# Kernel tuning notes

Measured on AMD Instinct MI355X. Metric: run time of the kernel, lower is better.

The kernel has to match this reference:

```python
import jax, jax.numpy as jnp
import numpy as np

B, CIN, CH, COUT = 16, 256, 256, 256
RES = 16
E = 32           # embed_dim
NEMB = 1024      # codebook size
NP = 128         # n_phylo_channels (ch - NP == NP)
L = 4            # n_phylolevels
K = 8            # attribute codes per level per kernel
KN = 32          # nonattribute codes per kernel (levels=1)
CP = L * K * E   # 1024 projected phylo channels
CN = KN * E      # 1024 projected nonattr channels
BETA = 0.25
EPS = 1e-5

def conv1x1(x, w, b):
    # x: [B,C,H,W], w: [O,C], b: [O]
    return jnp.einsum('oc,bchw->bohw', w, x) + b[None, :, None, None]

def layernorm_chw(x, w, b):
    # LayerNorm over (C,H,W) per sample, elementwise affine of shape [C,H,W]
    mu = jnp.mean(x, axis=(1, 2, 3), keepdims=True)
    var = jnp.var(x, axis=(1, 2, 3), keepdims=True)
    return (x - mu) * jax.lax.rsqrt(var + EPS) * w[None] + b[None]

def reshape_in(x, levels):
    # [B, E*levels*K', H, W] -> [B, E, K'*H*W, levels]
    Bb, C, H, W = x.shape
    Kp = C // (E * levels)
    x = x.reshape(Bb, E, levels, Kp, H * W)
    x = x.transpose(0, 1, 3, 4, 2)          # [B,E,K',HW,levels]
    return x.reshape(Bb, E, Kp * H * W, levels)

def reshape_out(x, levels):
    # [B, E, K'*HW, levels] -> [B, E*levels*K', RES, RES]
    Bb, Ee, N, Ll = x.shape
    Kp = N // (RES * RES)
    x = x.reshape(Bb, Ee, Kp, RES * RES, Ll)
    x = x.transpose(0, 1, 4, 2, 3)          # [B,E,levels,K',HW]
    return x.reshape(Bb, Ee * Ll * Kp, RES, RES)

def quantize(z, codebook):
    # z: [B, E, N, levels]; codebook: [NEMB, E]
    zp = z.transpose(0, 2, 3, 1)            # [B,N,levels,E]
    flat = zp.reshape(-1, E)
    d = (jnp.sum(flat * flat, axis=1, keepdims=True)
         - 2.0 * flat @ codebook.T
         + jnp.sum(codebook * codebook, axis=1)[None, :])
    idx = jnp.argmin(d, axis=1)
    zq = codebook[idx].reshape(zp.shape)
    sg = jax.lax.stop_gradient
    loss = jnp.mean((sg(zq) - zp) ** 2) + BETA * jnp.mean((zq - sg(zp)) ** 2)
    zq = zp + sg(zq - zp)                   # straight-through
    return zq.transpose(0, 3, 1, 2), loss

def setup_inputs() -> dict:
    key = jax.random.key(0)
    ks = jax.random.split(key, 20)
    s = 0.02
    inp = {
        'x': jax.random.normal(ks[0], (B, CIN, RES, RES), jnp.float32),
        'conv_in_w': jax.random.normal(ks[1], (CH, CIN), jnp.float32) * s,
        'conv_in_b': jnp.zeros((CH,), jnp.float32),
        'ln_p_w': jnp.ones((NP, RES, RES), jnp.float32),
        'ln_p_b': jnp.zeros((NP, RES, RES), jnp.float32),
        'wp_in': jax.random.normal(ks[2], (CP, NP), jnp.float32) * s,
        'bp_in': jnp.zeros((CP,), jnp.float32),
        'wp_out': jax.random.normal(ks[3], (NP, CP), jnp.float32) * s,
        'bp_out': jnp.zeros((NP,), jnp.float32),
        'ln_n_w': jnp.ones((CH - NP, RES, RES), jnp.float32),
        'ln_n_b': jnp.zeros((CH - NP, RES, RES), jnp.float32),
        'wn_in': jax.random.normal(ks[4], (CN, CH - NP), jnp.float32) * s,
        'bn_in': jnp.zeros((CN,), jnp.float32),
        'wn_out': jax.random.normal(ks[5], (CH - NP, CN), jnp.float32) * s,
        'bn_out': jnp.zeros((CH - NP,), jnp.float32),
        'codebook': jax.random.uniform(ks[6], (NEMB, E), jnp.float32,
                                       -1.0 / NEMB, 1.0 / NEMB),
        'conv_out_w': jax.random.normal(ks[7], (COUT, CH), jnp.float32) * s,
        'conv_out_b': jnp.zeros((COUT,), jnp.float32),
    }
    return inp

def reference(x, conv_in_w, conv_in_b, ln_p_w, ln_p_b, wp_in, bp_in,
              wp_out, bp_out, ln_n_w, ln_n_b, wn_in, bn_in, wn_out, bn_out,
              codebook, conv_out_w, conv_out_b):
    silu = jax.nn.silu
    h = conv1x1(silu(x), conv_in_w, conv_in_b)
    h_p, h_n = h[:, :NP], h[:, NP:]
    # phylo branch
    z_p = silu(conv1x1(layernorm_chw(silu(h_p), ln_p_w, ln_p_b), wp_in, bp_in))
    zq_p, loss_p = quantize(reshape_in(z_p, L), codebook)
    hout_p = silu(conv1x1(reshape_out(zq_p, L), wp_out, bp_out))
    # non-attribute branch (anticlassification path)
    z_n = silu(conv1x1(layernorm_chw(silu(h_n), ln_n_w, ln_n_b), wn_in, bn_in))
    zq_n, loss_n = quantize(reshape_in(z_n, 1), codebook)
    hout_n = silu(conv1x1(reshape_out(zq_n, 1), wn_out, bn_out))
    h_cat = jnp.concatenate([hout_p, hout_n], axis=1)
    out = conv1x1(silu(h_cat), conv_out_w, conv_out_b)
    return out, loss_p + loss_n, zq_p
```

## Files before the change

### kernel.cpp

```cpp
#include <hip/hip_runtime.h>
#include <hip/hip_bf16.h>


__device__ __forceinline__ float silu_rw(float x){ return x / (1.f + expf(-x)); }
__device__ __forceinline__ float b2f_rw(__hip_bfloat16 v){ return __bfloat162float(v); }
__device__ __forceinline__ float ldv_rw(const void* p, int i, int f32m){
  if (f32m) return ((const float*)p)[i];
  return b2f_rw(((const __hip_bfloat16*)p)[i]);
}

#define FLAGS_OFF 0
#define LOSS_OFF  4
#define STATS_OFF 8
#define CB32_OFF  128
#define CBN_OFF   32896
#define IDXP_OFF  33984
#define IDXN_OFF  165056
#define R2_OFF    296192
#define R3_OFF    820480
#define R1_OFF    1344768

__global__ __launch_bounds__(256) void detect_rw(const void* cbv, float* flags, float* lossacc){
  __shared__ int bad;
  if (threadIdx.x == 0) bad = 0;
  __syncthreads();
  const unsigned short* u = (const unsigned short*)cbv;
  int local = 0;
  for (int i = threadIdx.x; i < 32768; i += 256){
    unsigned e = (u[i] >> 7) & 0xFF;
    if (e >= 126) local = 1;
  }
  if (local) bad = 1;
  __syncthreads();
  if (threadIdx.x == 0){
    flags[0] = bad ? 1.f : 0.f;
    lossacc[0] = 0.f; lossacc[1] = 0.f;
  }
}

__global__ __launch_bounds__(256) void cbprep_rw(const void* cbv, const float* flags,
                                                 float* cb32, float* cbn){
  const int f32m = (flags[0] != 0.f);
  int j = blockIdx.x * 256 + threadIdx.x;
  if (j < 1024){
    float s = 0.f;
    for (int e = 0; e < 32; ++e){
      float v = ldv_rw(cbv, j*32 + e, f32m);
      cb32[j*32 + e] = v;
      s += v*v;
    }
    cbn[j] = s;
  }
}

template<int KCH, int INMODE, bool OUTSILU, bool ATOMIC, int LEVELS>
__global__ __launch_bounds__(256) void gemm2_rw(
    const float* __restrict__ inF, const float* __restrict__ inF2,
    const void* __restrict__ inV,
    const void* __restrict__ W, const void* __restrict__ biasO,
    const void* __restrict__ sbA, const void* __restrict__ sbB,
    const int* __restrict__ idxin, const float* __restrict__ cb32,
    float* __restrict__ outF, const float* __restrict__ flags,
    int KDIM, int OUTC, int o_off, int b_base, int ib_sub, int ob_sub)
{
  __shared__ float As[32][32];
  __shared__ float Bs[32][68];
  __shared__ int   IdxS[32][32];

  const int f32m = (flags[0] != 0.f);
  const int t  = threadIdx.x;
  const int q0 = (blockIdx.x << 5) + (b_base << 8);
  const int b  = q0 >> 8;
  const int p0 = q0 & 255;
  const int o0 = blockIdx.y << 6;
  const int k0base = blockIdx.z * KCH;
  const int tx = t & 15, ty = t >> 4;
  float acc[4][2] = {};

  const int sch = t >> 3, spx = (t & 7) << 2;

  if constexpr (INMODE == 3){
    #pragma unroll
    for (int j = 0; j < 4; ++j){
      const int p = p0 + spx + j;
      if constexpr (LEVELS == 4){
        const int l = sch >> 3, kp = sch & 7;
        IdxS[sch][spx + j] = idxin[b*8192 + (((kp << 8) + p) << 2) + l];
      } else {
        IdxS[sch][spx + j] = idxin[b*8192 + (sch << 8) + p];
      }
    }
    __syncthreads();
  }

  for (int kc = 0; kc < KCH; kc += 32){
    const int k0 = k0base + kc;
    if constexpr (INMODE == 0){
      const float4 v = *reinterpret_cast<const float4*>(
          &inF[(((b - ib_sub)*KDIM + k0 + sch) << 8) + p0 + spx]);
      *reinterpret_cast<float4*>(&As[sch][spx]) = v;
    } else if constexpr (INMODE == 2){
      if (f32m){
        const float* xf = (const float*)inV;
        float4 v = *reinterpret_cast<const float4*>(&xf[((b*KDIM + k0 + sch) << 8) + p0 + spx]);
        v.x = silu_rw(v.x); v.y = silu_rw(v.y); v.z = silu_rw(v.z); v.w = silu_rw(v.w);
        *reinterpret_cast<float4*>(&As[sch][spx]) = v;
      } else {
        const __hip_bfloat16* xb = (const __hip_bfloat16*)inV;
        const int off = ((b*KDIM + k0 + sch) << 8) + p0 + spx;
        #pragma unroll
        for (int j = 0; j < 4; ++j) As[sch][spx + j] = silu_rw(b2f_rw(xb[off + j]));
      }
    } else if constexpr (INMODE == 3){
      const int e = k0 >> 5;
      #pragma unroll
      for (int j = 0; j < 4; ++j)
        As[sch][spx + j] = cb32[((IdxS[sch][spx + j] & 1023) << 5) + e];
    } else {
      const float* src = (k0 < 128) ? inF : inF2;
      const void* sb   = (k0 < 128) ? sbA : sbB;
      const int kh = k0 & 127;
      const float bb = ldv_rw(sb, kh + sch, f32m);
      float4 v = *reinterpret_cast<const float4*>(&src[((b*128 + kh + sch) << 8) + p0 + spx]);
      v.x = silu_rw(v.x + bb); v.y = silu_rw(v.y + bb);
      v.z = silu_rw(v.z + bb); v.w = silu_rw(v.w + bb);
      *reinterpret_cast<float4*>(&As[sch][spx]) = v;
    }
    if (f32m){
      const float* Wf = (const float*)W;
      #pragma unroll
      for (int r = 0; r < 8; ++r){
        int ii = t + (r << 8); int oo = ii >> 5, cc = ii & 31;
        Bs[cc][oo] = Wf[(o0 + oo)*KDIM + k0 + cc];
      }
    } else {
      const __hip_bfloat16* Wb = (const __hip_bfloat16*)W;
      #pragma unroll
      for (int r = 0; r < 8; ++r){
        int ii = t + (r << 8); int oo = ii >> 5, cc = ii & 31;
        Bs[cc][oo] = b2f_rw(Wb[(o0 + oo)*KDIM + k0 + cc]);
      }
    }
    __syncthreads();
    #pragma unroll
    for (int kk = 0; kk < 32; ++kk){
      const float2 a = *reinterpret_cast<const float2*>(&As[kk][tx << 1]);
      const float4 w = *reinterpret_cast<const float4*>(&Bs[kk][ty << 2]);
      acc[0][0] += w.x*a.x; acc[0][1] += w.x*a.y;
      acc[1][0] += w.y*a.x; acc[1][1] += w.y*a.y;
      acc[2][0] += w.z*a.x; acc[2][1] += w.z*a.y;
      acc[3][0] += w.w*a.x; acc[3][1] += w.w*a.y;
    }
    __syncthreads();
  }
  #pragma unroll
  for (int i = 0; i < 4; ++i){
    const int o = o0 + (ty << 2) + i;
    const int base = (((b - ob_sub)*OUTC + o_off + o) << 8) + p0 + (tx << 1);
    if constexpr (ATOMIC){
      atomicAdd(&outF[base + 0], acc[i][0]);
      atomicAdd(&outF[base + 1], acc[i][1]);
    } else {
      const float bb = ldv_rw(biasO, o, f32m);
      float v0 = acc[i][0] + bb, v1 = acc[i][1] + bb;
      if constexpr (OUTSILU){ v0 = silu_rw(v0); v1 = silu_rw(v1); }
      *reinterpret_cast<float2*>(&outF[base]) = make_float2(v0, v1);
    }
  }
}

__global__ __launch_bounds__(256) void stats_rw(const float* __restrict__ h, float* __restrict__ stats){
  const int b = blockIdx.x >> 1, half = blockIdx.x & 1;
  const float* base = h + ((b*256 + half*128) << 8);
  float s = 0.f, s2 = 0.f;
  for (int i = threadIdx.x; i < 32768; i += 256){
    float a = silu_rw(base[i]);
    s += a; s2 += a*a;
  }
  __shared__ float sh[2][256];
  sh[0][threadIdx.x] = s; sh[1][threadIdx.x] = s2;
  __syncthreads();
  for (int st = 128; st > 0; st >>= 1){
    if (threadIdx.x < st){
      sh[0][threadIdx.x] += sh[0][threadIdx.x + st];
      sh[1][threadIdx.x] += sh[1][threadIdx.x + st];
    }
    __syncthreads();
  }
  if (threadIdx.x == 0){
    float mu  = sh[0][0] * (1.f/32768.f);
    float var = sh[1][0] * (1.f/32768.f) - mu*mu;
    stats[half*32 + b]      = mu;
    stats[half*32 + 16 + b] = 1.f / sqrtf(var + 1e-5f);
  }
}

__global__ __launch_bounds__(256) void ln_rw(const float* __restrict__ h,
    const void* lwp, const void* lbp, const void* lwn, const void* lbn,
    const float* __restrict__ stats, const float* __restrict__ flags,
    float* __restrict__ lnp, float* __restrict__ lnn){
  const int f32m = (flags[0] != 0.f);
  int i = blockIdx.x * 256 + threadIdx.x;
  int b = i >> 16, c = (i >> 8) & 255, p = i & 255;
  float a = silu_rw(h[i]);
  if (c < 128){
    float v = (a - stats[b]) * stats[16 + b] * ldv_rw(lwp, (c << 8) + p, f32m) + ldv_rw(lbp, (c << 8) + p, f32m);
    lnp[((b*128 + c) << 8) + p] = v;
  } else {
    int cc = c - 128;
    float v = (a - stats[32 + b]) * stats[48 + b] * ldv_rw(lwn, (cc << 8) + p, f32m) + ldv_rw(lbn, (cc << 8) + p, f32m);
    lnn[((b*128 + cc) << 8) + p] = v;
  }
}

template<int LEVELS>
__global__ __launch_bounds__(256) void quant_rw(const float* __restrict__ z,
    const float* __restrict__ cb32, const float* __restrict__ cbn,
    int* __restrict__ idxout, float* __restrict__ lossacc, int b_base, int CS){
  __shared__ float4 cbT[2056];
  __shared__ float  cbnS[1056];
  __shared__ float  red[256];

  const int tid = threadIdx.x;
  const int gid = blockIdx.x * 256 + tid;
  const int pt = gid & 7;
  const int vbase = gid >> 3;
  const int halfstride = CS << 12;
  const int vid0 = vbase, vid1 = vbase + halfstride;

  const int bl0 = vid0 >> 13, bl1 = vid1 >> 13;
  const int w = vid0 & 8191;
  int p, cbase;
  if (LEVELS == 4){
    int l = w & 3, n = w >> 2;
    p = n & 255; cbase = (l << 3) + (n >> 8);
  } else {
    p = w & 255; cbase = w >> 8;
  }

  #pragma unroll
  for (int q = 0; q < 4; ++q){
    const int i = tid + (q << 8);
    cbnS[i + (i >> 5)] = cbn[i];
  }

  float4 za[8], zb[8];
  float zn0 = 0.f, zn1 = 0.f;
  const int zoff = ((bl0 << 10) + cbase) << 8;
  const int zoff1 = ((bl1 << 10) + cbase) << 8;
  #pragma unroll
  for (int e4 = 0; e4 < 8; ++e4){
    float4 a, b;
    a.x = z[zoff  + (((e4<<2)+0) << 13) + p];
    a.y = z[zoff  + (((e4<<2)+1) << 13) + p];
    a.z = z[zoff  + (((e4<<2)+2) << 13) + p];
    a.w = z[zoff  + (((e4<<2)+3) << 13) + p];
    b.x = z[zoff1 + (((e4<<2)+0) << 13) + p];
    b.y = z[zoff1 + (((e4<<2)+1) << 13) + p];
    b.z = z[zoff1 + (((e4<<2)+2) << 13) + p];
    b.w = z[zoff1 + (((e4<<2)+3) << 13) + p];
    za[e4] = a; zb[e4] = b;
    zn0 += a.x*a.x; zn0 += a.y*a.y; zn0 += a.z*a.z; zn0 += a.w*a.w;
    zn1 += b.x*b.x; zn1 += b.y*b.y; zn1 += b.z*b.z; zn1 += b.w*b.w;
  }

  float best0 = __builtin_inff(), best1 = __builtin_inff();
  int bi0 = 0, bi1 = 0;

  const int jl0 = pt << 5;
  for (int t = 0; t < 4; ++t){
    __syncthreads();
    const float4* g4 = reinterpret_cast<const float4*>(cb32) + (t << 11);
    #pragma unroll
    for (int r = 0; r < 8; ++r){
      const int idx = tid + (r << 8);
      cbT[idx + (idx >> 8)] = g4[idx];
    }
    __syncthreads();

    #pragma unroll 4
    for (int i = 0; i < 32; ++i){
      const int jl = jl0 + i;
      const int j  = (t << 8) + jl;
      const float4* c = &cbT[(jl << 3) + (jl >> 5)];
      float dot0 = 0.f, dot1 = 0.f;
      #pragma unroll
      for (int e4 = 0; e4 < 8; ++e4){
        const float4 cc = c[e4];
        dot0 = fmaf(za[e4].x, cc.x, dot0); dot1 = fmaf(zb[e4].x, cc.x, dot1);
        dot0 = fmaf(za[e4].y, cc.y, dot0); dot1 = fmaf(zb[e4].y, cc.y, dot1);
        dot0 = fmaf(za[e4].z, cc.z, dot0); dot1 = fmaf(zb[e4].z, cc.z, dot1);
        dot0 = fmaf(za[e4].w, cc.w, dot0); dot1 = fmaf(zb[e4].w, cc.w, dot1);
      }
      const float cn = cbnS[j + (j >> 5)];
      const float d0 = (zn0 - 2.f*dot0) + cn;
      const float d1 = (zn1 - 2.f*dot1) + cn;
      if (d0 < best0){ best0 = d0; bi0 = j; }
      if (d1 < best1){ best1 = d1; bi1 = j; }
    }
  }

  #pragma unroll
  for (int k = 4; k > 0; k >>= 1){
    float od0 = __shfl_down(best0, k); int oj0 = __shfl_down(bi0, k);
    float od1 = __shfl_down(best1, k); int oj1 = __shfl_down(bi1, k);
    if (od0 < best0 || (od0 == best0 && oj0 < bi0)){ best0 = od0; bi0 = oj0; }
    if (od1 < best1 || (od1 == best1 && oj1 < bi1)){ best1 = od1; bi1 = oj1; }
  }
  if (pt == 0){
    idxout[(b_base + bl0)*8192 + w] = bi0;
    idxout[(b_base + bl1)*8192 + w] = bi1;
  }
  red[tid] = (pt == 0) ? (best0 + best1) : 0.f;
  __syncthreads();
  for (int st = 128; st > 0; st >>= 1){
    if (tid < st) red[tid] += red[tid + st];
    __syncthreads();
  }
  if (tid == 0) atomicAdd(lossacc, red[0]);
}

__global__ __launch_bounds__(256) void zqout_rw(const int* __restrict__ idxp,
    const float* __restrict__ cb32, float* __restrict__ out){
  int t = blockIdx.x * 256 + threadIdx.x;
  int l = t & 3, n = (t >> 2) & 2047, e = (t >> 13) & 31, b = t >> 18;
  int id = idxp[b*8192 + (n << 2) + l];
  out[t] = cb32[((id & 1023) << 5) + e];
}

__global__ __launch_bounds__(256) void zero_rw(float* __restrict__ p){
  p[blockIdx.x * 256 + threadIdx.x] = 0.f;
}

__global__ void loss_rw(const float* __restrict__ lossacc, float* __restrict__ out){
  if (threadIdx.x == 0 && blockIdx.x == 0)
    out[0] = 1.25f * (lossacc[0] + lossacc[1]) * (1.f/4194304.f);
}

extern "C" void kernel_launch(void* const* d_in, const int* in_sizes, int n_in,
                              void* d_out, int out_size, void* d_ws, size_t ws_size,
                              hipStream_t stream){
  (void)in_sizes; (void)n_in; (void)out_size;
  const void* x   = d_in[0];
  const void* ciw = d_in[1];
  const void* cib = d_in[2];
  const void* lwp = d_in[3];
  const void* lbp = d_in[4];
  const void* wpi = d_in[5];
  const void* bpi = d_in[6];
  const void* wpo = d_in[7];
  const void* bpo = d_in[8];
  const void* lwn = d_in[9];
  const void* lbn = d_in[10];
  const void* wni = d_in[11];
  const void* bni = d_in[12];
  const void* wno = d_in[13];
  const void* bno = d_in[14];
  const void* cbk = d_in[15];
  const void* cow = d_in[16];
  const void* cob = d_in[17];

  float* ws    = (float*)d_ws;
  float* flags = ws + FLAGS_OFF;
  float* loss  = ws + LOSS_OFF;
  float* stats = ws + STATS_OFF;
  float* cb32  = ws + CB32_OFF;
  float* cbn   = ws + CBN_OFF;
  int*   idxp  = (int*)(ws + IDXP_OFF);
  int*   idxn  = (int*)(ws + IDXN_OFF);
  float* R2    = ws + R2_OFF;
  float* R3    = ws + R3_OFF;
  float* R1    = ws + R1_OFF;

  float* outO = (float*)d_out;
  float* outL = outO + 1048576;
  float* outZ = outO + 1048577;

  const size_t wsf = ws_size / 4;
  int CS = 4;
  if      (wsf >= (size_t)R1_OFF + 16u*262144u) CS = 16;
  else if (wsf >= (size_t)R1_OFF +  8u*262144u) CS = 8;

  detect_rw<<<1, 256, 0, stream>>>(cbk, flags, loss);
  cbprep_rw<<<4, 256, 0, stream>>>(cbk, flags, cb32, cbn);
  gemm2_rw<256,2,false,false,0><<<dim3(128,4), 256, 0, stream>>>(
      nullptr, nullptr, x, ciw, cib, nullptr, nullptr, nullptr, nullptr,
      R1, flags, 256, 256, 0, 0, 0, 0);
  stats_rw<<<32, 256, 0, stream>>>(R1, stats);
  ln_rw<<<4096, 256, 0, stream>>>(R1, lwp, lbp, lwn, lbn, stats, flags, R2, R3);
  for (int c = 0; c < 16; c += CS){
    gemm2_rw<128,0,true,false,0><<<dim3(CS*8,16), 256, 0, stream>>>(
        R2, nullptr, nullptr, wpi, bpi, nullptr, nullptr, nullptr, nullptr,
        R1, flags, 128, 1024, 0, c, 0, c);
    quant_rw<4><<<CS*128, 256, 0, stream>>>(R1, cb32, cbn, idxp, loss + 0, c, CS);
  }
  for (int c = 0; c < 16; c += CS){
    gemm2_rw<128,0,true,false,0><<<dim3(CS*8,16), 256, 0, stream>>>(
        R3, nullptr, nullptr, wni, bni, nullptr, nullptr, nullptr, nullptr,
        R1, flags, 128, 1024, 0, c, 0, c);
    quant_rw<1><<<CS*128, 256, 0, stream>>>(R1, cb32, cbn, idxn, loss + 1, c, CS);
  }
  zqout_rw<<<16384, 256, 0, stream>>>(idxp, cb32, outZ);
  zero_rw<<<4096, 256, 0, stream>>>(R2);
  gemm2_rw<256,3,false,true,4><<<dim3(128,2,4), 256, 0, stream>>>(
      nullptr, nullptr, nullptr, wpo, nullptr, nullptr, nullptr, idxp, cb32,
      R2, flags, 1024, 128, 0, 0, 0, 0);
  gemm2_rw<256,3,false,true,1><<<dim3(128,2,4), 256, 0, stream>>>(
      nullptr, nullptr, nullptr, wno, nullptr, nullptr, nullptr, idxn, cb32,
      R3, flags, 1024, 128, 0, 0, 0, 0);
  gemm2_rw<256,5,false,false,0><<<dim3(128,4), 256, 0, stream>>>(
      R2, R3, nullptr, cow, cob, bpo, bno, nullptr, nullptr,
      outO, flags, 256, 256, 0, 0, 0, 0);
  loss_rw<<<1, 64, 0, stream>>>(loss, outL);
}
```

Before: 630.2 us.

## Use output buffer as full-batch scratch and quantize four vectors per thread

The projected activations for all 16 samples are now written into the output buffer, which is free at that point, so the workspace-size-dependent chunk loop over batches goes away and each branch runs as one GEMM plus one quantize launch. The quantize kernel now keeps four input vectors per thread in registers instead of two, so each codebook entry read from shared memory feeds twice as many FMAs. The cost is much higher register pressure in the quantize kernel, which may lower occupancy. The scheme also depends on the output region not being written until the quantize kernels have finished with it.

```diff
diff --git a/kernel.cpp b/kernel.cpp
--- a/kernel.cpp
+++ b/kernel.cpp
@@ -2,11 +2,11 @@
 #include <hip/hip_bf16.h>
 
 
-__device__ __forceinline__ float silu_rw(float x){ return x / (1.f + expf(-x)); }
-__device__ __forceinline__ float b2f_rw(__hip_bfloat16 v){ return __bfloat162float(v); }
-__device__ __forceinline__ float ldv_rw(const void* p, int i, int f32m){
+__device__ __forceinline__ float silu_rx(float x){ return x / (1.f + expf(-x)); }
+__device__ __forceinline__ float b2f_rx(__hip_bfloat16 v){ return __bfloat162float(v); }
+__device__ __forceinline__ float ldv_rx(const void* p, int i, int f32m){
   if (f32m) return ((const float*)p)[i];
-  return b2f_rw(((const __hip_bfloat16*)p)[i]);
+  return b2f_rx(((const __hip_bfloat16*)p)[i]);
 }
 
 #define FLAGS_OFF 0
@@ -20,7 +20,7 @@
 #define R3_OFF    820480
 #define R1_OFF    1344768
 
-__global__ __launch_bounds__(256) void detect_rw(const void* cbv, float* flags, float* lossacc){
+__global__ __launch_bounds__(256) void detect_rx(const void* cbv, float* flags, float* lossacc){
   __shared__ int bad;
   if (threadIdx.x == 0) bad = 0;
   __syncthreads();
@@ -38,14 +38,14 @@
   }
 }
 
-__global__ __launch_bounds__(256) void cbprep_rw(const void* cbv, const float* flags,
+__global__ __launch_bounds__(256) void cbprep_rx(const void* cbv, const float* flags,
                                                  float* cb32, float* cbn){
   const int f32m = (flags[0] != 0.f);
   int j = blockIdx.x * 256 + threadIdx.x;
   if (j < 1024){
     float s = 0.f;
     for (int e = 0; e < 32; ++e){
-      float v = ldv_rw(cbv, j*32 + e, f32m);
+      float v = ldv_rx(cbv, j*32 + e, f32m);
       cb32[j*32 + e] = v;
       s += v*v;
     }
@@ -54,14 +54,14 @@
 }
 
 template<int KCH, int INMODE, bool OUTSILU, bool ATOMIC, int LEVELS>
-__global__ __launch_bounds__(256) void gemm2_rw(
+__global__ __launch_bounds__(256) void gemm2_rx(
     const float* __restrict__ inF, const float* __restrict__ inF2,
     const void* __restrict__ inV,
     const void* __restrict__ W, const void* __restrict__ biasO,
     const void* __restrict__ sbA, const void* __restrict__ sbB,
     const int* __restrict__ idxin, const float* __restrict__ cb32,
     float* __restrict__ outF, const float* __restrict__ flags,
-    int KDIM, int OUTC, int o_off, int b_base, int ib_sub, int ob_sub)
+    int KDIM, int OUTC)
 {
   __shared__ float As[32][32];
   __shared__ float Bs[32][68];
@@ -69,7 +69,7 @@
 
   const int f32m = (flags[0] != 0.f);
   const int t  = threadIdx.x;
-  const int q0 = (blockIdx.x << 5) + (b_base << 8);
+  const int q0 = blockIdx.x << 5;
   const int b  = q0 >> 8;
   const int p0 = q0 & 255;
   const int o0 = blockIdx.y << 6;
@@ -97,19 +97,19 @@
     const int k0 = k0base + kc;
     if constexpr (INMODE == 0){
       const float4 v = *reinterpret_cast<const float4*>(
-          &inF[(((b - ib_sub)*KDIM + k0 + sch) << 8) + p0 + spx]);
+          &inF[((b*KDIM + k0 + sch) << 8) + p0 + spx]);
       *reinterpret_cast<float4*>(&As[sch][spx]) = v;
     } else if constexpr (INMODE == 2){
       if (f32m){
         const float* xf = (const float*)inV;
         float4 v = *reinterpret_cast<const float4*>(&xf[((b*KDIM + k0 + sch) << 8) + p0 + spx]);
-        v.x = silu_rw(v.x); v.y = silu_rw(v.y); v.z = silu_rw(v.z); v.w = silu_rw(v.w);
+        v.x = silu_rx(v.x); v.y = silu_rx(v.y); v.z = silu_rx(v.z); v.w = silu_rx(v.w);
         *reinterpret_cast<float4*>(&As[sch][spx]) = v;
       } else {
         const __hip_bfloat16* xb = (const __hip_bfloat16*)inV;
         const int off = ((b*KDIM + k0 + sch) << 8) + p0 + spx;
         #pragma unroll
-        for (int j = 0; j < 4; ++j) As[sch][spx + j] = silu_rw(b2f_rw(xb[off + j]));
+        for (int j = 0; j < 4; ++j) As[sch][spx + j] = silu_rx(b2f_rx(xb[off + j]));
       }
     } else if constexpr (INMODE == 3){
       const int e = k0 >> 5;
@@ -120,10 +120,10 @@
       const float* src = (k0 < 128) ? inF : inF2;
       const void* sb   = (k0 < 128) ? sbA : sbB;
       const int kh = k0 & 127;
-      const float bb = ldv_rw(sb, kh + sch, f32m);
+      const float bb = ldv_rx(sb, kh + sch, f32m);
       float4 v = *reinterpret_cast<const float4*>(&src[((b*128 + kh + sch) << 8) + p0 + spx]);
-      v.x = silu_rw(v.x + bb); v.y = silu_rw(v.y + bb);
-      v.z = silu_rw(v.z + bb); v.w = silu_rw(v.w + bb);
+      v.x = silu_rx(v.x + bb); v.y = silu_rx(v.y + bb);
+      v.z = silu_rx(v.z + bb); v.w = silu_rx(v.w + bb);
       *reinterpret_cast<float4*>(&As[sch][spx]) = v;
     }
     if (f32m){
@@ -138,7 +138,7 @@
       #pragma unroll
       for (int r = 0; r < 8; ++r){
         int ii = t + (r << 8); int oo = ii >> 5, cc = ii & 31;
-        Bs[cc][oo] = b2f_rw(Wb[(o0 + oo)*KDIM + k0 + cc]);
+        Bs[cc][oo] = b2f_rx(Wb[(o0 + oo)*KDIM + k0 + cc]);
       }
     }
     __syncthreads();
@@ -156,25 +156,25 @@
   #pragma unroll
   for (int i = 0; i < 4; ++i){
     const int o = o0 + (ty << 2) + i;
-    const int base = (((b - ob_sub)*OUTC + o_off + o) << 8) + p0 + (tx << 1);
+    const int base = ((b*OUTC + o) << 8) + p0 + (tx << 1);
     if constexpr (ATOMIC){
       atomicAdd(&outF[base + 0], acc[i][0]);
       atomicAdd(&outF[base + 1], acc[i][1]);
     } else {
-      const float bb = ldv_rw(biasO, o, f32m);
+      const float bb = ldv_rx(biasO, o, f32m);
       float v0 = acc[i][0] + bb, v1 = acc[i][1] + bb;
-      if constexpr (OUTSILU){ v0 = silu_rw(v0); v1 = silu_rw(v1); }
+      if constexpr (OUTSILU){ v0 = silu_rx(v0); v1 = silu_rx(v1); }
       *reinterpret_cast<float2*>(&outF[base]) = make_float2(v0, v1);
     }
   }
 }
 
-__global__ __launch_bounds__(256) void stats_rw(const float* __restrict__ h, float* __restrict__ stats){
+__global__ __launch_bounds__(256) void stats_rx(const float* __restrict__ h, float* __restrict__ stats){
   const int b = blockIdx.x >> 1, half = blockIdx.x & 1;
   const float* base = h + ((b*256 + half*128) << 8);
   float s = 0.f, s2 = 0.f;
   for (int i = threadIdx.x; i < 32768; i += 256){
-    float a = silu_rw(base[i]);
+    float a = silu_rx(base[i]);
     s += a; s2 += a*a;
   }
   __shared__ float sh[2][256];
@@ -195,28 +195,28 @@
   }
 }
 
-__global__ __launch_bounds__(256) void ln_rw(const float* __restrict__ h,
+__global__ __launch_bounds__(256) void ln_rx(const float* __restrict__ h,
     const void* lwp, const void* lbp, const void* lwn, const void* lbn,
     const float* __restrict__ stats, const float* __restrict__ flags,
     float* __restrict__ lnp, float* __restrict__ lnn){
   const int f32m = (flags[0] != 0.f);
   int i = blockIdx.x * 256 + threadIdx.x;
   int b = i >> 16, c = (i >> 8) & 255, p = i & 255;
-  float a = silu_rw(h[i]);
+  float a = silu_rx(h[i]);
   if (c < 128){
-    float v = (a - stats[b]) * stats[16 + b] * ldv_rw(lwp, (c << 8) + p, f32m) + ldv_rw(lbp, (c << 8) + p, f32m);
+    float v = (a - stats[b]) * stats[16 + b] * ldv_rx(lwp, (c << 8) + p, f32m) + ldv_rx(lbp, (c << 8) + p, f32m);
     lnp[((b*128 + c) << 8) + p] = v;
   } else {
     int cc = c - 128;
-    float v = (a - stats[32 + b]) * stats[48 + b] * ldv_rw(lwn, (cc << 8) + p, f32m) + ldv_rw(lbn, (cc << 8) + p, f32m);
+    float v = (a - stats[32 + b]) * stats[48 + b] * ldv_rx(lwn, (cc << 8) + p, f32m) + ldv_rx(lbn, (cc << 8) + p, f32m);
     lnn[((b*128 + cc) << 8) + p] = v;
   }
 }
 
 template<int LEVELS>
-__global__ __launch_bounds__(256) void quant_rw(const float* __restrict__ z,
+__global__ __launch_bounds__(256) void quant_rx(const float* __restrict__ z,
     const float* __restrict__ cb32, const float* __restrict__ cbn,
-    int* __restrict__ idxout, float* __restrict__ lossacc, int b_base, int CS){
+    int* __restrict__ idxout, float* __restrict__ lossacc){
   __shared__ float4 cbT[2056];
   __shared__ float  cbnS[1056];
   __shared__ float  red[256];
@@ -225,11 +225,8 @@
   const int gid = blockIdx.x * 256 + tid;
   const int pt = gid & 7;
   const int vbase = gid >> 3;
-  const int halfstride = CS << 12;
-  const int vid0 = vbase, vid1 = vbase + halfstride;
-
-  const int bl0 = vid0 >> 13, bl1 = vid1 >> 13;
-  const int w = vid0 & 8191;
+
+  const int w = vbase & 8191;
   int p, cbase;
   if (LEVELS == 4){
     int l = w & 3, n = w >> 2;
@@ -244,28 +241,30 @@
     cbnS[i + (i >> 5)] = cbn[i];
   }
 
-  float4 za[8], zb[8];
-  float zn0 = 0.f, zn1 = 0.f;
-  const int zoff = ((bl0 << 10) + cbase) << 8;
-  const int zoff1 = ((bl1 << 10) + cbase) << 8;
+  int blk[4];
+  float4 zv[4][8];
+  float zn[4];
   #pragma unroll
-  for (int e4 = 0; e4 < 8; ++e4){
-    float4 a, b;
-    a.x = z[zoff  + (((e4<<2)+0) << 13) + p];
-    a.y = z[zoff  + (((e4<<2)+1) << 13) + p];
-    a.z = z[zoff  + (((e4<<2)+2) << 13) + p];
-    a.w = z[zoff  + (((e4<<2)+3) << 13) + p];
-    b.x = z[zoff1 + (((e4<<2)+0) << 13) + p];
-    b.y = z[zoff1 + (((e4<<2)+1) << 13) + p];
-    b.z = z[zoff1 + (((e4<<2)+2) << 13) + p];
-    b.w = z[zoff1 + (((e4<<2)+3) << 13) + p];
-    za[e4] = a; zb[e4] = b;
-    zn0 += a.x*a.x; zn0 += a.y*a.y; zn0 += a.z*a.z; zn0 += a.w*a.w;
-    zn1 += b.x*b.x; zn1 += b.y*b.y; zn1 += b.z*b.z; zn1 += b.w*b.w;
-  }
-
-  float best0 = __builtin_inff(), best1 = __builtin_inff();
-  int bi0 = 0, bi1 = 0;
+  for (int k = 0; k < 4; ++k){
+    const int vid = vbase + (k << 15);
+    blk[k] = vid >> 13;
+    const int zoff = ((blk[k] << 10) + cbase) << 8;
+    float zs = 0.f;
+    #pragma unroll
+    for (int e4 = 0; e4 < 8; ++e4){
+      float4 a;
+      a.x = z[zoff + (((e4<<2)+0) << 13) + p];
+      a.y = z[zoff + (((e4<<2)+1) << 13) + p];
+      a.z = z[zoff + (((e4<<2)+2) << 13) + p];
+      a.w = z[zoff + (((e4<<2)+3) << 13) + p];
+      zv[k][e4] = a;
+      zs += a.x*a.x; zs += a.y*a.y; zs += a.z*a.z; zs += a.w*a.w;
+    }
+    zn[k] = zs;
+  }
+
+  float best[4] = {__builtin_inff(), __builtin_inff(), __builtin_inff(), __builtin_inff()};
+  int bi[4] = {0, 0, 0, 0};
 
   const int jl0 = pt << 5;
   for (int t = 0; t < 4; ++t){
@@ -278,40 +277,49 @@
     }
     __syncthreads();
 
-    #pragma unroll 4
+    #pragma unroll 2
     for (int i = 0; i < 32; ++i){
       const int jl = jl0 + i;
       const int j  = (t << 8) + jl;
       const float4* c = &cbT[(jl << 3) + (jl >> 5)];
-      float dot0 = 0.f, dot1 = 0.f;
+      float dot0 = 0.f, dot1 = 0.f, dot2 = 0.f, dot3 = 0.f;
       #pragma unroll
       for (int e4 = 0; e4 < 8; ++e4){
         const float4 cc = c[e4];
-        dot0 = fmaf(za[e4].x, cc.x, dot0); dot1 = fmaf(zb[e4].x, cc.x, dot1);
-        dot0 = fmaf(za[e4].y, cc.y, dot0); dot1 = fmaf(zb[e4].y, cc.y, dot1);
-        dot0 = fmaf(za[e4].z, cc.z, dot0); dot1 = fmaf(zb[e4].z, cc.z, dot1);
-        dot0 = fmaf(za[e4].w, cc.w, dot0); dot1 = fmaf(zb[e4].w, cc.w, dot1);
+        dot0 = fmaf(zv[0][e4].x, cc.x, dot0); dot1 = fmaf(zv[1][e4].x, cc.x, dot1);
+        dot2 = fmaf(zv[2][e4].x, cc.x, dot2); dot3 = fmaf(zv[3][e4].x, cc.x, dot3);
+        dot0 = fmaf(zv[0][e4].y, cc.y, dot0); dot1 = fmaf(zv[1][e4].y, cc.y, dot1);
+        dot2 = fmaf(zv[2][e4].y, cc.y, dot2); dot3 = fmaf(zv[3][e4].y, cc.y, dot3);
+        dot0 = fmaf(zv[0][e4].z, cc.z, dot0); dot1 = fmaf(zv[1][e4].z, cc.z, dot1);
+        dot2 = fmaf(zv[2][e4].z, cc.z, dot2); dot3 = fmaf(zv[3][e4].z, cc.z, dot3);
+        dot0 = fmaf(zv[0][e4].w, cc.w, dot0); dot1 = fmaf(zv[1][e4].w, cc.w, dot1);
+        dot2 = fmaf(zv[2][e4].w, cc.w, dot2); dot3 = fmaf(zv[3][e4].w, cc.w, dot3);
       }
       const float cn = cbnS[j + (j >> 5)];
-      const float d0 = (zn0 - 2.f*dot0) + cn;
-      const float d1 = (zn1 - 2.f*dot1) + cn;
-      if (d0 < best0){ best0 = d0; bi0 = j; }
-      if (d1 < best1){ best1 = d1; bi1 = j; }
+      const float d0 = (zn[0] - 2.f*dot0) + cn;
+      const float d1 = (zn[1] - 2.f*dot1) + cn;
+      const float d2 = (zn[2] - 2.f*dot2) + cn;
+      const float d3 = (zn[3] - 2.f*dot3) + cn;
+      if (d0 < best[0]){ best[0] = d0; bi[0] = j; }
+      if (d1 < best[1]){ best[1] = d1; bi[1] = j; }
+      if (d2 < best[2]){ best[2] = d2; bi[2] = j; }
+      if (d3 < best[3]){ best[3] = d3; bi[3] = j; }
     }
   }
 
   #pragma unroll
   for (int k = 4; k > 0; k >>= 1){
-    float od0 = __shfl_down(best0, k); int oj0 = __shfl_down(bi0, k);
-    float od1 = __shfl_down(best1, k); int oj1 = __shfl_down(bi1, k);
-    if (od0 < best0 || (od0 == best0 && oj0 < bi0)){ best0 = od0; bi0 = oj0; }
-    if (od1 < best1 || (od1 == best1 && oj1 < bi1)){ best1 = od1; bi1 = oj1; }
+    #pragma unroll
+    for (int v = 0; v < 4; ++v){
+      float od = __shfl_down(best[v], k); int oj = __shfl_down(bi[v], k);
+      if (od < best[v] || (od == best[v] && oj < bi[v])){ best[v] = od; bi[v] = oj; }
+    }
   }
   if (pt == 0){
-    idxout[(b_base + bl0)*8192 + w] = bi0;
-    idxout[(b_base + bl1)*8192 + w] = bi1;
-  }
-  red[tid] = (pt == 0) ? (best0 + best1) : 0.f;
+    #pragma unroll
+    for (int v = 0; v < 4; ++v) idxout[blk[v]*8192 + w] = bi[v];
+  }
+  red[tid] = (pt == 0) ? (best[0] + best[1] + best[2] + best[3]) : 0.f;
   __syncthreads();
   for (int st = 128; st > 0; st >>= 1){
     if (tid < st) red[tid] += red[tid + st];
@@ -320,7 +328,7 @@
   if (tid == 0) atomicAdd(lossacc, red[0]);
 }
 
-__global__ __launch_bounds__(256) void zqout_rw(const int* __restrict__ idxp,
+__global__ __launch_bounds__(256) void zqout_rx(const int* __restrict__ idxp,
     const float* __restrict__ cb32, float* __restrict__ out){
   int t = blockIdx.x * 256 + threadIdx.x;
   int l = t & 3, n = (t >> 2) & 2047, e = (t >> 13) & 31, b = t >> 18;
@@ -328,11 +336,11 @@
   out[t] = cb32[((id & 1023) << 5) + e];
 }
 
-__global__ __launch_bounds__(256) void zero_rw(float* __restrict__ p){
+__global__ __launch_bounds__(256) void zero_rx(float* __restrict__ p){
   p[blockIdx.x * 256 + threadIdx.x] = 0.f;
 }
 
-__global__ void loss_rw(const float* __restrict__ lossacc, float* __restrict__ out){
+__global__ void loss_rx(const float* __restrict__ lossacc, float* __restrict__ out){
   if (threadIdx.x == 0 && blockIdx.x == 0)
     out[0] = 1.25f * (lossacc[0] + lossacc[1]) * (1.f/4194304.f);
 }
@@ -340,7 +348,7 @@
 extern "C" void kernel_launch(void* const* d_in, const int* in_sizes, int n_in,
                               void* d_out, int out_size, void* d_ws, size_t ws_size,
                               hipStream_t stream){
-  (void)in_sizes; (void)n_in; (void)out_size;
+  (void)in_sizes; (void)n_in; (void)out_size; (void)ws_size;
   const void* x   = d_in[0];
   const void* ciw = d_in[1];
   const void* cib = d_in[2];
@@ -375,41 +383,33 @@
   float* outO = (float*)d_out;
   float* outL = outO + 1048576;
   float* outZ = outO + 1048577;
-
-  const size_t wsf = ws_size / 4;
-  int CS = 4;
-  if      (wsf >= (size_t)R1_OFF + 16u*262144u) CS = 16;
-  else if (wsf >= (size_t)R1_OFF +  8u*262144u) CS = 8;
-
-  detect_rw<<<1, 256, 0, stream>>>(cbk, flags, loss);
-  cbprep_rw<<<4, 256, 0, stream>>>(cbk, flags, cb32, cbn);
-  gemm2_rw<256,2,false,false,0><<<dim3(128,4), 256, 0, stream>>>(
+  float* zbuf = outO;
+
+  detect_rx<<<1, 256, 0, stream>>>(cbk, flags, loss);
+  cbprep_rx<<<4, 256, 0, stream>>>(cbk, flags, cb32, cbn);
+  gemm2_rx<256,2,false,false,0><<<dim3(128,4), 256, 0, stream>>>(
       nullptr, nullptr, x, ciw, cib, nullptr, nullptr, nullptr, nullptr,
-      R1, flags, 256, 256, 0, 0, 0, 0);
-  stats_rw<<<32, 256, 0, stream>>>(R1, stats);
-  ln_rw<<<4096, 256, 0, stream>>>(R1, lwp, lbp, lwn, lbn, stats, flags, R2, R3);
-  for (int c = 0; c < 16; c += CS){
-    gemm2_rw<128,0,true,false,0><<<dim3(CS*8,16), 256, 0, stream>>>(
-        R2, nullptr, nullptr, wpi, bpi, nullptr, nullptr, nullptr, nullptr,
-        R1, flags, 128, 1024, 0, c, 0, c);
-    quant_rw<4><<<CS*128, 256, 0, stream>>>(R1, cb32, cbn, idxp, loss + 0, c, CS);
-  }
-  for (int c = 0; c < 16; c += CS){
-    gemm2_rw<128,0,true,false,0><<<dim3(CS*8,16), 256, 0, stream>>>(
-        R3, nullptr, nullptr, wni, bni, nullptr, nullptr, nullptr, nullptr,
-        R1, flags, 128, 1024, 0, c, 0, c);
-    quant_rw<1><<<CS*128, 256, 0, stream>>>(R1, cb32, cbn, idxn, loss + 1, c, CS);
-  }
-  zqout_rw<<<16384, 256, 0, stream>>>(idxp, cb32, outZ);
-  zero_rw<<<4096, 256, 0, stream>>>(R2);
-  gemm2_rw<256,3,false,true,4><<<dim3(128,2,4), 256, 0, stream>>>(
+      R1, flags, 256, 256);
+  stats_rx<<<32, 256, 0, stream>>>(R1, stats);
+  ln_rx<<<4096, 256, 0, stream>>>(R1, lwp, lbp, lwn, lbn, stats, flags, R2, R3);
+  gemm2_rx<128,0,true,false,0><<<dim3(128,16), 256, 0, stream>>>(
+      R2, nullptr, nullptr, wpi, bpi, nullptr, nullptr, nullptr, nullptr,
+      zbuf, flags, 128, 1024);
+  quant_rx<4><<<1024, 256, 0, stream>>>(zbuf, cb32, cbn, idxp, loss + 0);
+  gemm2_rx<128,0,true,false,0><<<dim3(128,16), 256, 0, stream>>>(
+      R3, nullptr, nullptr, wni, bni, nullptr, nullptr, nullptr, nullptr,
+      zbuf, flags, 128, 1024);
+  quant_rx<1><<<1024, 256, 0, stream>>>(zbuf, cb32, cbn, idxn, loss + 1);
+  zqout_rx<<<16384, 256, 0, stream>>>(idxp, cb32, outZ);
+  zero_rx<<<4096, 256, 0, stream>>>(R2);
+  gemm2_rx<256,3,false,true,4><<<dim3(128,2,4), 256, 0, stream>>>(
       nullptr, nullptr, nullptr, wpo, nullptr, nullptr, nullptr, idxp, cb32,
-      R2, flags, 1024, 128, 0, 0, 0, 0);
-  gemm2_rw<256,3,false,true,1><<<dim3(128,2,4), 256, 0, stream>>>(
+      R2, flags, 1024, 128);
+  gemm2_rx<256,3,false,true,1><<<dim3(128,2,4), 256, 0, stream>>>(
       nullptr, nullptr, nullptr, wno, nullptr, nullptr, nullptr, idxn, cb32,
-      R3, flags, 1024, 128, 0, 0, 0, 0);
-  gemm2_rw<256,5,false,false,0><<<dim3(128,4), 256, 0, stream>>>(
+      R3, flags, 1024, 128);
+  gemm2_rx<256,5,false,false,0><<<dim3(128,4), 256, 0, stream>>>(
       R2, R3, nullptr, cow, cob, bpo, bno, nullptr, nullptr,
-      outO, flags, 256, 256, 0, 0, 0, 0);
-  loss_rw<<<1, 64, 0, stream>>>(loss, outL);
-}
+      outO, flags, 256, 256);
+  loss_rx<<<1, 64, 0, stream>>>(loss, outL);
+}
```

Result: no change. 637.9 us (+1.2%).
